# Kernel tuning notes

Hardware: AMD Instinct MI355X
Metric: run time of the kernel (lower is better)

Reference implementation:

```python
import jax, jax.numpy as jnp
import numpy as np

B, A, C = 128, 8732, 21

def setup_inputs() -> dict:
    key = jax.random.key(0)
    k1, k2, k3, k4 = jax.random.split(key, 4)
    return {
        "location_output": jax.random.normal(k1, (B, A, 4), dtype=jnp.float32),
        "classifi_output": jax.random.normal(k2, (B, A, C), dtype=jnp.float32),
        "location_label": jax.random.normal(k3, (B, A, 4), dtype=jnp.float32),
        "classifi_label": jax.random.randint(k4, (B, A), 0, C, dtype=jnp.int64),
    }

def reference(location_output, classifi_output, location_label, classifi_label):
    mask = classifi_label > 0                      # [B, A] positive anchors
    pos_num = mask.sum(axis=1)                     # [B]

    # SmoothL1 (beta=1), summed over the 4 box coords, masked to positives
    diff = location_output - location_label
    ad = jnp.abs(diff)
    sl1 = jnp.where(ad < 1.0, 0.5 * diff * diff, ad - 0.5).sum(axis=-1)  # [B, A]
    loc_loss = (sl1 * mask.astype(sl1.dtype)).sum(axis=-1)               # [B]

    # Per-anchor cross entropy
    logp = jax.nn.log_softmax(classifi_output, axis=-1)                  # [B, A, C]
    con = -jnp.take_along_axis(logp, classifi_label[..., None], axis=-1)[..., 0]  # [B, A]

    # Hard negative mining: rank negatives by CE (descending), keep top 3*pos_num
    con_neg = jnp.where(mask, 0.0, con)
    rank = jnp.argsort(jnp.argsort(-con_neg, axis=1), axis=1)            # rank in descending order
    neg_num = jnp.minimum(3 * pos_num, A)
    neg_num = jnp.where(neg_num == 0, 3, neg_num)
    neg_mask = rank < neg_num[:, None]

    con_loss = (con * (mask.astype(con.dtype) + neg_mask.astype(con.dtype))).sum(axis=1)  # [B]

    total = loc_loss + con_loss
    denom = jnp.where(pos_num != 0, pos_num, 1).astype(total.dtype)
    return (total / denom).mean()
```

## Files before the change

### kernel.cpp

```cpp
#include <hip/hip_runtime.h>

#define NBATCH 128
#define NANCH  8732
#define NCLS   21
#define SUBS   8
#define SUBLEN 1092
#define ROUNDS 5


__device__ __forceinline__ float waveReduceF(float v) {
    #pragma unroll
    for (int o = 32; o > 0; o >>= 1) v += __shfl_down(v, o, 64);
    return v;
}
__device__ __forceinline__ unsigned waveReduceU(unsigned v) {
    #pragma unroll
    for (int o = 32; o > 0; o >>= 1) v += __shfl_down(v, o, 64);
    return v;
}

__device__ __forceinline__ float con_from_row(const float* __restrict__ row, int lbl) {
    float m = row[0];
    #pragma unroll
    for (int c = 1; c < NCLS; ++c) m = fmaxf(m, row[c]);
    float s = 0.f;
    #pragma unroll
    for (int c = 0; c < NCLS; ++c) s += __expf(row[c] - m);
    return m + __logf(s) - row[lbl];
}

__global__ __launch_bounds__(256) void anchor_kernel(
    const float*  __restrict__ loc_out,
    const float*  __restrict__ cls_out,
    const float*  __restrict__ loc_lab,
    const int*    __restrict__ labels,
    float4* __restrict__ partial)
{
    const int bid  = blockIdx.x;
    const int b    = bid >> 3;
    const int sub  = bid & 7;
    const int tid  = threadIdx.x;
    const int start = sub * SUBLEN;
    const int len   = (sub == 7) ? (NANCH - 7 * SUBLEN) : SUBLEN;

    float loc_s = 0.f, all_s = 0.f, pos_s = 0.f;
    unsigned pc = 0;

    #pragma unroll
    for (int r = 0; r < ROUNDS; ++r) {
        const int al = r * 256 + tid;
        if (al < len) {
            const size_t ba = (size_t)b * NANCH + start + al;
            const float* __restrict__ row = cls_out + ba * NCLS;

            const float4 r0 = *(const float4*)(row +  0);
            const float4 r1 = *(const float4*)(row +  4);
            const float4 r2 = *(const float4*)(row +  8);
            const float4 r3 = *(const float4*)(row + 12);
            const float4 r4 = *(const float4*)(row + 16);
            const float  r5 = row[20];

            const int lbl = labels[ba];
            const float4 lo4 = ((const float4*)loc_out)[ba];
            const float4 ll4 = ((const float4*)loc_lab)[ba];

            float m = r0.x;
            m = fmaxf(m, r0.y); m = fmaxf(m, r0.z); m = fmaxf(m, r0.w);
            m = fmaxf(m, r1.x); m = fmaxf(m, r1.y); m = fmaxf(m, r1.z); m = fmaxf(m, r1.w);
            m = fmaxf(m, r2.x); m = fmaxf(m, r2.y); m = fmaxf(m, r2.z); m = fmaxf(m, r2.w);
            m = fmaxf(m, r3.x); m = fmaxf(m, r3.y); m = fmaxf(m, r3.z); m = fmaxf(m, r3.w);
            m = fmaxf(m, r4.x); m = fmaxf(m, r4.y); m = fmaxf(m, r4.z); m = fmaxf(m, r4.w);
            m = fmaxf(m, r5);

            float s = __expf(r0.x - m) + __expf(r0.y - m) + __expf(r0.z - m) + __expf(r0.w - m)
                    + __expf(r1.x - m) + __expf(r1.y - m) + __expf(r1.z - m) + __expf(r1.w - m)
                    + __expf(r2.x - m) + __expf(r2.y - m) + __expf(r2.z - m) + __expf(r2.w - m)
                    + __expf(r3.x - m) + __expf(r3.y - m) + __expf(r3.z - m) + __expf(r3.w - m)
                    + __expf(r4.x - m) + __expf(r4.y - m) + __expf(r4.z - m) + __expf(r4.w - m)
                    + __expf(r5 - m);

            float tgt = r0.x;
            tgt = (lbl ==  1) ? r0.y : tgt;  tgt = (lbl ==  2) ? r0.z : tgt;
            tgt = (lbl ==  3) ? r0.w : tgt;  tgt = (lbl ==  4) ? r1.x : tgt;
            tgt = (lbl ==  5) ? r1.y : tgt;  tgt = (lbl ==  6) ? r1.z : tgt;
            tgt = (lbl ==  7) ? r1.w : tgt;  tgt = (lbl ==  8) ? r2.x : tgt;
            tgt = (lbl ==  9) ? r2.y : tgt;  tgt = (lbl == 10) ? r2.z : tgt;
            tgt = (lbl == 11) ? r2.w : tgt;  tgt = (lbl == 12) ? r3.x : tgt;
            tgt = (lbl == 13) ? r3.y : tgt;  tgt = (lbl == 14) ? r3.z : tgt;
            tgt = (lbl == 15) ? r3.w : tgt;  tgt = (lbl == 16) ? r4.x : tgt;
            tgt = (lbl == 17) ? r4.y : tgt;  tgt = (lbl == 18) ? r4.z : tgt;
            tgt = (lbl == 19) ? r4.w : tgt;  tgt = (lbl == 20) ? r5   : tgt;

            const float con = m + __logf(s) - tgt;
            all_s += con;
            if (lbl > 0) {
                pos_s += con;
                pc++;
                float d0 = lo4.x - ll4.x, d1 = lo4.y - ll4.y,
                      d2 = lo4.z - ll4.z, d3 = lo4.w - ll4.w;
                float a0 = fabsf(d0), a1 = fabsf(d1), a2 = fabsf(d2), a3 = fabsf(d3);
                loc_s += ((a0 < 1.f) ? 0.5f * d0 * d0 : (a0 - 0.5f))
                       + ((a1 < 1.f) ? 0.5f * d1 * d1 : (a1 - 0.5f))
                       + ((a2 < 1.f) ? 0.5f * d2 * d2 : (a2 - 0.5f))
                       + ((a3 < 1.f) ? 0.5f * d3 * d3 : (a3 - 0.5f));
            }
        }
    }

    loc_s = waveReduceF(loc_s);
    all_s = waveReduceF(all_s);
    pos_s = waveReduceF(pos_s);
    pc    = waveReduceU(pc);

    __shared__ float sL[4], sA[4], sP[4];
    __shared__ unsigned sC[4];
    const int w = tid >> 6, lane = tid & 63;
    if (lane == 0) { sL[w] = loc_s; sA[w] = all_s; sP[w] = pos_s; sC[w] = pc; }
    __syncthreads();
    if (tid == 0) {
        float L = sL[0] + sL[1] + sL[2] + sL[3];
        float S = sA[0] + sA[1] + sA[2] + sA[3];
        float P = sP[0] + sP[1] + sP[2] + sP[3];
        unsigned C = sC[0] + sC[1] + sC[2] + sC[3];
        partial[bid] = make_float4(L, S, P, (float)C);
    }
}

__global__ __launch_bounds__(256) void finalize_kernel(
    const float* __restrict__ cls_out,
    const int*   __restrict__ labels,
    const float4* __restrict__ partial,
    float* __restrict__ out)
{
    const int tid = threadIdx.x;

    __shared__ float sLoc[NBATCH], sPos[NBATCH], sCnt[NBATCH], sConl[NBATCH];
    __shared__ unsigned sK[NBATCH];
    __shared__ unsigned nflag;
    if (tid == 0) nflag = 0;
    __syncthreads();

    if (tid < NBATCH) {
        float loc = 0.f, all = 0.f, pos = 0.f, cnt = 0.f;
        #pragma unroll
        for (int c = 0; c < SUBS; ++c) {
            float4 p = partial[tid * SUBS + c];
            loc += p.x; all += p.y; pos += p.z; cnt += p.w;
        }
        unsigned k = 3u * (unsigned)cnt;
        if (k > NANCH) k = NANCH;
        if (k == 0u) k = 3u;
        sLoc[tid] = loc; sPos[tid] = pos; sCnt[tid] = cnt;
        sConl[tid] = all + pos;
        if (k < NANCH) { sK[tid] = k; atomicAdd(&nflag, 1u); }
        else sK[tid] = 0u;
    }
    __syncthreads();

    if (nflag) {
        __shared__ float    rF[256];
        __shared__ unsigned rU[256];
        for (int b2 = 0; b2 < NBATCH; ++b2) {
            unsigned k = sK[b2];
            if (!k) continue;

            auto count_gt = [&](float t) -> unsigned {
                unsigned cc = 0;
                for (int an = tid; an < NANCH; an += 256) {
                    size_t ba = (size_t)b2 * NANCH + an;
                    int lbl = labels[ba];
                    if (lbl > 0) continue;
                    float con = con_from_row(cls_out + ba * NCLS, lbl);
                    if (con > t) cc++;
                }
                rU[tid] = cc; __syncthreads();
                for (int o = 128; o > 0; o >>= 1) {
                    if (tid < o) rU[tid] += rU[tid + o];
                    __syncthreads();
                }
                unsigned r = rU[0]; __syncthreads();
                return r;
            };

            unsigned cpos = count_gt(0.0f);
            float negpart = 0.f;

            if (k <= cpos) {
                unsigned lo = 0u, hi = 0x7F800000u;
                while (hi - lo > 1u) {
                    unsigned mid = lo + (hi - lo) / 2u;
                    unsigned cc = count_gt(__uint_as_float(mid));
                    if (cc >= k) lo = mid; else hi = mid;
                }
                float v = __uint_as_float(hi);
                float ss = 0.f; unsigned c1 = 0;
                for (int an = tid; an < NANCH; an += 256) {
                    size_t ba = (size_t)b2 * NANCH + an;
                    int lbl = labels[ba];
                    if (lbl > 0) continue;
                    float con = con_from_row(cls_out + ba * NCLS, lbl);
                    if (con > v) { ss += con; c1++; }
                }
                rF[tid] = ss; rU[tid] = c1; __syncthreads();
                for (int o = 128; o > 0; o >>= 1) {
                    if (tid < o) { rF[tid] += rF[tid + o]; rU[tid] += rU[tid + o]; }
                    __syncthreads();
                }
                negpart = rF[0] + (float)(k - rU[0]) * v;
                __syncthreads();
            } else {
                if (tid == 0) {
                    float np = 0.f;
                    unsigned mrem = k - cpos;
                    for (int an = 0; an < NANCH; ++an) {
                        size_t ba = (size_t)b2 * NANCH + an;
                        int lbl = labels[ba];
                        float con = con_from_row(cls_out + ba * NCLS, lbl);
                        float cneg = (lbl > 0) ? 0.f : con;
                        if (cneg > 0.f) np += con;
                        else if (mrem > 0u) { np += con; mrem--; }
                    }
                    rF[0] = np;
                }
                __syncthreads();
                negpart = rF[0];
                __syncthreads();
            }

            if (tid == 0) sConl[b2] = sPos[b2] + negpart;
            __syncthreads();
        }
    }

    float t = 0.f;
    if (tid < NBATCH) {
        float denom = (sCnt[tid] != 0.f) ? sCnt[tid] : 1.f;
        t = (sLoc[tid] + sConl[tid]) / denom;
    }
    t = waveReduceF(t);
    __shared__ float sW[4];
    const int w = tid >> 6, lane = tid & 63;
    if (lane == 0) sW[w] = t;
    __syncthreads();
    if (tid == 0) out[0] = (sW[0] + sW[1] + sW[2] + sW[3]) * (1.f / NBATCH);
}

extern "C" void kernel_launch(void* const* d_in, const int* in_sizes, int n_in,
                              void* d_out, int out_size, void* d_ws, size_t ws_size,
                              hipStream_t stream) {
    const float* loc_out = (const float*)d_in[0];
    const float* cls_out = (const float*)d_in[1];
    const float* loc_lab = (const float*)d_in[2];
    const int*   labels  = (const int*)d_in[3];
    float* out = (float*)d_out;
    float4* partial = (float4*)d_ws;

    anchor_kernel<<<NBATCH * SUBS, 256, 0, stream>>>(loc_out, cls_out, loc_lab, labels, partial);
    finalize_kernel<<<1, 256, 0, stream>>>(cls_out, labels, partial, out);
}
```

Measured before the change: 176.8 us.

## Stage classification rows through LDS with direct global-to-LDS loads

Replaces per-thread strided float4 loads of 21-float rows, which are misaligned because the row stride is 84 bytes, with coalesced block-wide global_load_lds copies of each 256-anchor chunk into shared memory. Each thread then reads its row from LDS. The goal is fully coalesced, aligned global traffic in place of unaligned per-thread vector loads. In exchange it adds two barriers per round, LDS bank conflicts from the stride-21 row reads, and about 21 KB of LDS per block, which may lower occupancy.

```diff
diff --git a/kernel.cpp b/kernel.cpp
--- a/kernel.cpp
+++ b/kernel.cpp
@@ -27,6 +27,13 @@
     #pragma unroll
     for (int c = 0; c < NCLS; ++c) s += __expf(row[c] - m);
     return m + __logf(s) - row[lbl];
+}
+
+__device__ __forceinline__ void gload_lds16(const float4* g, float4* l) {
+    __builtin_amdgcn_global_load_lds(
+        (const __attribute__((address_space(1))) void*)g,
+        (__attribute__((address_space(3))) void*)l,
+        16, 0, 0);
 }
 
 __global__ __launch_bounds__(256) void anchor_kernel(
@@ -36,61 +43,60 @@
     const int*    __restrict__ labels,
     float4* __restrict__ partial)
 {
+    __shared__ float ldsrow[256 * NCLS];
+
     const int bid  = blockIdx.x;
     const int b    = bid >> 3;
     const int sub  = bid & 7;
     const int tid  = threadIdx.x;
     const int start = sub * SUBLEN;
     const int len   = (sub == 7) ? (NANCH - 7 * SUBLEN) : SUBLEN;
+    const int wbase = (tid >> 6) << 6;
 
     float loc_s = 0.f, all_s = 0.f, pos_s = 0.f;
     unsigned pc = 0;
 
-    #pragma unroll
     for (int r = 0; r < ROUNDS; ++r) {
-        const int al = r * 256 + tid;
-        if (al < len) {
+        const int al    = r * 256 + tid;
+        const bool valid = al < len;
+        const int nA    = min(256, len - r * 256);
+        const int nF4   = (nA * NCLS) >> 2;
+
+        const size_t rbase = ((size_t)b * NANCH + start + r * 256) * NCLS;
+        const float4* gsrc = reinterpret_cast<const float4*>(cls_out + rbase);
+
+        int lbl = 0; float4 lo4 = {}; float4 ll4 = {};
+        if (valid) {
             const size_t ba = (size_t)b * NANCH + start + al;
-            const float* __restrict__ row = cls_out + ba * NCLS;
-
-            const float4 r0 = *(const float4*)(row +  0);
-            const float4 r1 = *(const float4*)(row +  4);
-            const float4 r2 = *(const float4*)(row +  8);
-            const float4 r3 = *(const float4*)(row + 12);
-            const float4 r4 = *(const float4*)(row + 16);
-            const float  r5 = row[20];
-
-            const int lbl = labels[ba];
-            const float4 lo4 = ((const float4*)loc_out)[ba];
-            const float4 ll4 = ((const float4*)loc_lab)[ba];
-
-            float m = r0.x;
-            m = fmaxf(m, r0.y); m = fmaxf(m, r0.z); m = fmaxf(m, r0.w);
-            m = fmaxf(m, r1.x); m = fmaxf(m, r1.y); m = fmaxf(m, r1.z); m = fmaxf(m, r1.w);
-            m = fmaxf(m, r2.x); m = fmaxf(m, r2.y); m = fmaxf(m, r2.z); m = fmaxf(m, r2.w);
-            m = fmaxf(m, r3.x); m = fmaxf(m, r3.y); m = fmaxf(m, r3.z); m = fmaxf(m, r3.w);
-            m = fmaxf(m, r4.x); m = fmaxf(m, r4.y); m = fmaxf(m, r4.z); m = fmaxf(m, r4.w);
-            m = fmaxf(m, r5);
-
-            float s = __expf(r0.x - m) + __expf(r0.y - m) + __expf(r0.z - m) + __expf(r0.w - m)
-                    + __expf(r1.x - m) + __expf(r1.y - m) + __expf(r1.z - m) + __expf(r1.w - m)
-                    + __expf(r2.x - m) + __expf(r2.y - m) + __expf(r2.z - m) + __expf(r2.w - m)
-                    + __expf(r3.x - m) + __expf(r3.y - m) + __expf(r3.z - m) + __expf(r3.w - m)
-                    + __expf(r4.x - m) + __expf(r4.y - m) + __expf(r4.z - m) + __expf(r4.w - m)
-                    + __expf(r5 - m);
-
-            float tgt = r0.x;
-            tgt = (lbl ==  1) ? r0.y : tgt;  tgt = (lbl ==  2) ? r0.z : tgt;
-            tgt = (lbl ==  3) ? r0.w : tgt;  tgt = (lbl ==  4) ? r1.x : tgt;
-            tgt = (lbl ==  5) ? r1.y : tgt;  tgt = (lbl ==  6) ? r1.z : tgt;
-            tgt = (lbl ==  7) ? r1.w : tgt;  tgt = (lbl ==  8) ? r2.x : tgt;
-            tgt = (lbl ==  9) ? r2.y : tgt;  tgt = (lbl == 10) ? r2.z : tgt;
-            tgt = (lbl == 11) ? r2.w : tgt;  tgt = (lbl == 12) ? r3.x : tgt;
-            tgt = (lbl == 13) ? r3.y : tgt;  tgt = (lbl == 14) ? r3.z : tgt;
-            tgt = (lbl == 15) ? r3.w : tgt;  tgt = (lbl == 16) ? r4.x : tgt;
-            tgt = (lbl == 17) ? r4.y : tgt;  tgt = (lbl == 18) ? r4.z : tgt;
-            tgt = (lbl == 19) ? r4.w : tgt;  tgt = (lbl == 20) ? r5   : tgt;
-
+            lbl = labels[ba];
+            lo4 = ((const float4*)loc_out)[ba];
+            ll4 = ((const float4*)loc_lab)[ba];
+        }
+
+        if (r) __syncthreads();
+        float4* lbase = (float4*)ldsrow;
+        #pragma unroll
+        for (int i = 0; i < 6; ++i) {
+            const int idx = i * 256 + tid;
+            if (idx < nF4)
+                gload_lds16(gsrc + idx, lbase + i * 256 + wbase);
+        }
+        __syncthreads();
+
+        if (valid) {
+            const float* __restrict__ row = ldsrow + tid * NCLS;
+            float f[NCLS];
+            #pragma unroll
+            for (int c = 0; c < NCLS; ++c) f[c] = row[c];
+
+            float m = f[0];
+            #pragma unroll
+            for (int c = 1; c < NCLS; ++c) m = fmaxf(m, f[c]);
+            float s = 0.f;
+            #pragma unroll
+            for (int c = 0; c < NCLS; ++c) s += __expf(f[c] - m);
+
+            const float tgt = row[lbl];
             const float con = m + __logf(s) - tgt;
             all_s += con;
             if (lbl > 0) {
```

After: 176.5 us. Within noise of the previous version (-0.2%).
